# Kernel optimization log

Measured on AMD Instinct MI355X. Metric: run time of the kernel, lower is better.

Reference implementation:

```python
import jax, jax.numpy as jnp
import numpy as np

B, S, D, H = 2, 2048, 1024, 16
DK = D // H
NEG = -1e9


def setup_inputs() -> dict:
    key = jax.random.key(0)
    ks = jax.random.split(key, 12)
    sc = 1.0 / np.sqrt(D)
    inp = {
        "query": jax.random.normal(ks[0], (B, S, D), jnp.float32),
        "key": jax.random.normal(ks[1], (B, S, D), jnp.float32),
        "value": jax.random.normal(ks[2], (B, S, D), jnp.float32),
        "mask": jnp.ones((B, 1, S), jnp.int32),
        "Wq": jax.random.normal(ks[3], (D, D), jnp.float32) * sc,
        "bq": jnp.zeros((D,), jnp.float32),
        "Wk": jax.random.normal(ks[4], (D, D), jnp.float32) * sc,
        "bk": jnp.zeros((D,), jnp.float32),
        "Wv": jax.random.normal(ks[5], (D, D), jnp.float32) * sc,
        "bv": jnp.zeros((D,), jnp.float32),
        "Wo": jax.random.normal(ks[6], (D, D), jnp.float32) * sc,
        "bo": jnp.zeros((D,), jnp.float32),
    }
    return inp


def reference(query, key, value, mask, Wq, bq, Wk, bk, Wv, bv, Wo, bo):
    # projections + split heads: [B,S,D] -> [B,H,S,DK]
    def proj(x, W, b):
        return (x @ W + b).reshape(B, S, H, DK).transpose(0, 2, 1, 3)

    q = proj(query, Wq, bq)
    k = proj(key, Wk, bk)
    v = proj(value, Wv, bv)

    scores = jnp.einsum("bhqd,bhkd->bhqk", q, k) / jnp.sqrt(jnp.float32(DK))
    # mask: [B,1,S] -> unsqueeze head dim -> [B,1,1,S], broadcast over heads & queries
    m = mask[:, None, :, :]  # [B,1,1,S]
    scores = jnp.where(m == 0, NEG, scores)
    p_attn = jax.nn.softmax(scores, axis=-1)  # dropout p=0 (eval)
    x = jnp.einsum("bhqk,bhkd->bhqd", p_attn, v)
    x = x.transpose(0, 2, 1, 3).reshape(B, S, D)
    return x @ Wo + bo
```

## Files before the change

kernel.cpp:

```cpp
#include <hip/hip_runtime.h>
#include <stdint.h>

typedef unsigned short u16;
typedef __bf16 bf16x8 __attribute__((ext_vector_type(8), may_alias));
typedef unsigned short u16x8 __attribute__((ext_vector_type(8), may_alias));
typedef unsigned short u16x4 __attribute__((ext_vector_type(4), may_alias));
typedef float f32x4 __attribute__((ext_vector_type(4)));
typedef float f32x16 __attribute__((ext_vector_type(16)));

__device__ __forceinline__ u16 f2bf(float f) {
    union { float f; uint32_t i; } v; v.f = f;
    return (u16)((v.i + 0x7FFFu + ((v.i >> 16) & 1u)) >> 16);
}

__device__ __forceinline__ float exp2_hw(float x) {
#if __has_builtin(__builtin_amdgcn_exp2f)
    return __builtin_amdgcn_exp2f(x);
#else
    float r; asm("v_exp_f32 %0, %1" : "=v"(r) : "v"(x)); return r;
#endif
}

__device__ __forceinline__ uint32_t cvt_pk_bf16(float a, float b) {
    uint32_t r;
    asm("v_cvt_pk_bf16_f32 %0, %1, %2" : "=v"(r) : "v"(a), "v"(b));
    return r;
}

__device__ __forceinline__ void gld_lds16(const u16* g, u16* l) {
    __builtin_amdgcn_global_load_lds(
        (const __attribute__((address_space(1))) unsigned int*)g,
        (__attribute__((address_space(3))) unsigned int*)l, 16, 0, 0);
}

__global__ __launch_bounds__(256) void cvt_all(
    const float* __restrict__ s0, const float* __restrict__ s1, const float* __restrict__ s2,
    const float* __restrict__ w0, const float* __restrict__ w1,
    const float* __restrict__ w2, const float* __restrict__ w3,
    u16* __restrict__ d0, u16* __restrict__ d1, u16* __restrict__ d2,
    u16* __restrict__ t0, u16* __restrict__ t1,
    u16* __restrict__ t2, u16* __restrict__ t3)
{
    __shared__ float L[64][65];
    const int z = blockIdx.z;
    const int tid = threadIdx.x;
    if (z < 3) {
        const float* s = (z == 0) ? s0 : (z == 1) ? s1 : s2;
        u16*         d = (z == 0) ? d0 : (z == 1) ? d1 : d2;
        const size_t base = ((size_t)blockIdx.x * 256 + tid) * 16;
        #pragma unroll
        for (int p = 0; p < 2; ++p) {
            float4 a = *reinterpret_cast<const float4*>(s + base + p * 8);
            float4 b = *reinterpret_cast<const float4*>(s + base + p * 8 + 4);
            u16x8 o;
            o[0] = f2bf(a.x); o[1] = f2bf(a.y); o[2] = f2bf(a.z); o[3] = f2bf(a.w);
            o[4] = f2bf(b.x); o[5] = f2bf(b.y); o[6] = f2bf(b.z); o[7] = f2bf(b.w);
            *reinterpret_cast<u16x8*>(d + base + p * 8) = o;
        }
    } else {
        if (blockIdx.x >= 256) return;
        const int zi = z - 3;
        const float* w = (zi == 0) ? w0 : (zi == 1) ? w1 : (zi == 2) ? w2 : w3;
        u16*         t = (zi == 0) ? t0 : (zi == 1) ? t1 : (zi == 2) ? t2 : t3;
        const int k0 = (blockIdx.x & 15) * 64, n0 = (blockIdx.x >> 4) * 64;
        const int rr = tid >> 6, cc = tid & 63;
        #pragma unroll
        for (int p = 0; p < 16; ++p)
            L[p * 4 + rr][cc] = w[(size_t)(k0 + p * 4 + rr) * 1024 + n0 + cc];
        __syncthreads();
        #pragma unroll
        for (int p = 0; p < 16; ++p)
            t[(size_t)(n0 + p * 4 + rr) * 1024 + k0 + cc] = f2bf(L[cc][p * 4 + rr]);
    }
}

__global__ __launch_bounds__(256) void gemm_bt(
    const u16* __restrict__ A0, const u16* __restrict__ A1, const u16* __restrict__ A2,
    const u16* __restrict__ B0, const u16* __restrict__ B1, const u16* __restrict__ B2,
    const float* __restrict__ c0, const float* __restrict__ c1, const float* __restrict__ c2,
    void* __restrict__ d0, void* __restrict__ d1, void* __restrict__ d2,
    int mode_override)
{
    __shared__ u16 As[2 * 4096];
    __shared__ u16 Bs[2 * 4096];

    const int z = blockIdx.z;
    const u16* A = (z == 0) ? A0 : (z == 1) ? A1 : A2;
    const u16* BT = (z == 0) ? B0 : (z == 1) ? B1 : B2;
    const float* bias = (z == 0) ? c0 : (z == 1) ? c1 : c2;
    void* dst = (z == 0) ? d0 : (z == 1) ? d1 : d2;
    const int mode = (mode_override >= 0) ? mode_override : ((z == 2) ? 2 : 0);

    const int tid  = threadIdx.x;
    const int wave = tid >> 6, lane = tid & 63;
    const int quad = lane >> 4, l15 = lane & 15;
    const int row0 = blockIdx.x * 128, col0 = blockIdx.y * 128;
    const int wrow = (wave >> 1) * 64, wcol = (wave & 1) * 64;

    const int sidx0 = tid, sidx1 = 256 + tid;
    const int sr0 = sidx0 >> 2, sc0 = ((sidx0 & 3) ^ ((sr0 >> 1) & 3)) * 8;
    const int sr1 = sidx1 >> 2, sc1 = ((sidx1 & 3) ^ ((sr1 >> 1) & 3)) * 8;
    const size_t aoff0 = (size_t)(row0 + sr0) * 1024 + sc0;
    const size_t aoff1 = (size_t)(row0 + sr1) * 1024 + sc1;
    const size_t boff0 = (size_t)(col0 + sr0) * 1024 + sc0;
    const size_t boff1 = (size_t)(col0 + sr1) * 1024 + sc1;
    u16* const asl0 = &As[(size_t)(wave * 64) * 8];
    u16* const asl1 = &As[(size_t)(256 + wave * 64) * 8];
    u16* const bsl0 = &Bs[(size_t)(wave * 64) * 8];
    u16* const bsl1 = &Bs[(size_t)(256 + wave * 64) * 8];

    f32x4 acc[4][4] = {};

    gld_lds16(A + aoff0, asl0);
    gld_lds16(BT + boff0, bsl0);
    gld_lds16(A + aoff1, asl1);
    gld_lds16(BT + boff1, bsl1);
    __syncthreads();

    int cur = 0;
    for (int k0 = 0; k0 < 1024; k0 += 32) {
        if (k0 < 992) {
            const int nb = (cur ^ 1) * 4096;
            gld_lds16(A + aoff0 + (k0 + 32), asl0 + nb);
            gld_lds16(BT + boff0 + (k0 + 32), bsl0 + nb);
            gld_lds16(A + aoff1 + (k0 + 32), asl1 + nb);
            gld_lds16(BT + boff1 + (k0 + 32), bsl1 + nb);
        }

        const u16* Ab = &As[cur * 4096];
        const u16* Bb = &Bs[cur * 4096];
        bf16x8 a[4], b[4];
        #pragma unroll
        for (int i = 0; i < 4; ++i) {
            const int ar = wrow + i * 16 + l15;
            a[i] = *reinterpret_cast<const bf16x8*>(&Ab[ar * 32 + (quad ^ ((ar >> 1) & 3)) * 8]);
        }
        #pragma unroll
        for (int j = 0; j < 4; ++j) {
            const int br = wcol + j * 16 + l15;
            b[j] = *reinterpret_cast<const bf16x8*>(&Bb[br * 32 + (quad ^ ((br >> 1) & 3)) * 8]);
        }
        #pragma unroll
        for (int i = 0; i < 4; ++i)
            #pragma unroll
            for (int j = 0; j < 4; ++j)
                acc[i][j] = __builtin_amdgcn_mfma_f32_16x16x32_bf16(a[i], b[j], acc[i][j], 0, 0, 0);

        __syncthreads();
        cur ^= 1;
    }

    const float emul = (mode == 0 && z == 0 && mode_override < 0) ? 0.18033688011112042f : 1.0f;

    #pragma unroll
    for (int i = 0; i < 4; ++i) {
        #pragma unroll
        for (int j = 0; j < 4; ++j) {
            const int gc  = col0 + wcol + j * 16 + l15;
            const float bv = bias[gc];
            const int gr0 = row0 + wrow + i * 16 + quad * 4;
            if (mode == 3) {
                float* df = (float*)dst;
                #pragma unroll
                for (int r = 0; r < 4; ++r)
                    df[(size_t)(gr0 + r) * 1024 + gc] = acc[i][j][r] + bv;
            } else if (mode == 2) {
                u16* dp = (u16*)dst;
                const int b = gr0 >> 11, s = gr0 & 2047;
                const int h = gc >> 6,  dk = gc & 63;
                u16x4 pk;
                pk[0] = f2bf(acc[i][j][0] + bv);
                pk[1] = f2bf(acc[i][j][1] + bv);
                pk[2] = f2bf(acc[i][j][2] + bv);
                pk[3] = f2bf(acc[i][j][3] + bv);
                *reinterpret_cast<u16x4*>(dp + ((size_t)((b * 16 + h) * 64 + dk)) * 2048 + s) = pk;
            } else {
                u16* dp = (u16*)dst;
                #pragma unroll
                for (int r = 0; r < 4; ++r) {
                    const int gr = gr0 + r;
                    const int b = gr >> 11, s = gr & 2047;
                    const int h = gc >> 6, dk = gc & 63;
                    dp[((size_t)((b * 16 + h) * 2048 + s)) * 64 + dk] = f2bf((acc[i][j][r] + bv) * emul);
                }
            }
        }
    }
}

__global__ __launch_bounds__(512, 4) void attn_fused(
    const u16* __restrict__ Qb, const u16* __restrict__ Kb,
    const u16* __restrict__ Vt, const int* __restrict__ mask,
    u16* __restrict__ ctx)
{
    __shared__ __align__(16) u16 SMEM[16896];

    const int tid  = threadIdx.x;
    const int w    = tid >> 6;
    const int lane = tid & 63;
    const int l31  = lane & 31;
    const int hi   = lane >> 5;
    const int qw   = w & 3;
    const int kh   = w >> 2;

    const int id = blockIdx.x;
    const int sw = (id & 7) * 64 + (id >> 3);
    const int bh = sw >> 4;
    const int q0 = (sw & 15) * 128;
    const int b  = bh >> 4, h = bh & 15;

    const u16* Qp = Qb + (size_t)bh * 2048 * 64;
    const u16* Kp = Kb + (size_t)bh * 2048 * 64;
    const u16* Vp = Vt + (size_t)bh * 64 * 2048;
    const int* mp = mask + b * 2048;

    bf16x8 qf[4];
    {
        const u16* qrow = Qp + (size_t)(q0 + qw * 32 + l31) * 64 + hi * 8;
        #pragma unroll
        for (int s = 0; s < 4; ++s)
            qf[s] = *reinterpret_cast<const bf16x8*>(qrow + s * 16);
    }

    const int scb = tid & 7, sr = tid >> 3;
    const u16* kg0 = Kp + (size_t)sr * 64 + scb * 8;
    const u16* vg0 = Vp + (size_t)sr * 2048 + scb * 8;
    const int dK = scb * 512 + (sr ^ scb) * 8;

    {
        u16x8 kr = *reinterpret_cast<const u16x8*>(kg0);
        u16x8 vr = *reinterpret_cast<const u16x8*>(vg0);
        *reinterpret_cast<u16x8*>(&SMEM[dK])        = kr;
        *reinterpret_cast<u16x8*>(&SMEM[4096 + dK]) = vr;
    }
    int mreg = mp[lane];
    __syncthreads();

    f32x16 accO0 = {}, accO1 = {};
    float la0 = 0.f, la1 = 0.f, la2 = 0.f, la3 = 0.f;
    const int paddr = (lane ^ 32) << 2;

    int cur = 0;
    for (int t = 0; t < 32; ++t) {
        const int kk = t * 64;
        u16x8 krn, vrn; int mnext = 1;
        if (t < 31) {
            krn = *reinterpret_cast<const u16x8*>(kg0 + (size_t)(kk + 64) * 64);
            vrn = *reinterpret_cast<const u16x8*>(vg0 + (kk + 64));
            mnext = mp[kk + 64 + lane];
        }
        const u16* Kb_ = &SMEM[cur * 8192];
        const u16* Vb_ = &SMEM[cur * 8192 + 4096];

        const bool fullmask = (__ballot(mreg != 0) == ~0ull);

        f32x16 z = {};
        #pragma unroll
        for (int s = 0; s < 4; ++s) {
            const int cb = s * 2 + hi;
            const bf16x8 ak = *reinterpret_cast<const bf16x8*>(
                &Kb_[cb * 512 + (((kh * 32 + l31)) ^ cb) * 8]);
            z = __builtin_amdgcn_mfma_f32_32x32x16_bf16(ak, qf[s], z, 0, 0, 0);
        }
        float p[16];
        #pragma unroll
        for (int r = 0; r < 16; ++r) p[r] = exp2_hw(z[r]);
        if (!fullmask) {
            #pragma unroll
            for (int r = 0; r < 16; ++r) {
                const int kv = kk + kh * 32 + (r & 3) + 8 * (r >> 2) + 4 * hi;
                if (mp[kv] == 0) p[r] = 0.f;
            }
        }
        la0 += p[0] + p[4] + p[8]  + p[12];
        la1 += p[1] + p[5] + p[9]  + p[13];
        la2 += p[2] + p[6] + p[10] + p[14];
        la3 += p[3] + p[7] + p[11] + p[15];

        const uint32_t wd0 = cvt_pk_bf16(p[0],  p[1]);
        const uint32_t wd1 = cvt_pk_bf16(p[2],  p[3]);
        const uint32_t wd2 = cvt_pk_bf16(p[4],  p[5]);
        const uint32_t wd3 = cvt_pk_bf16(p[6],  p[7]);
        const uint32_t wd4 = cvt_pk_bf16(p[8],  p[9]);
        const uint32_t wd5 = cvt_pk_bf16(p[10], p[11]);
        const uint32_t wd6 = cvt_pk_bf16(p[12], p[13]);
        const uint32_t wd7 = cvt_pk_bf16(p[14], p[15]);
        const uint32_t s0 = hi ? wd0 : wd2;
        const uint32_t s1 = hi ? wd1 : wd3;
        const uint32_t s2 = hi ? wd4 : wd6;
        const uint32_t s3 = hi ? wd5 : wd7;
        const uint32_t r0 = (uint32_t)__builtin_amdgcn_ds_bpermute(paddr, (int)s0);
        const uint32_t r1 = (uint32_t)__builtin_amdgcn_ds_bpermute(paddr, (int)s1);
        const uint32_t r2 = (uint32_t)__builtin_amdgcn_ds_bpermute(paddr, (int)s2);
        const uint32_t r3 = (uint32_t)__builtin_amdgcn_ds_bpermute(paddr, (int)s3);
        union { uint32_t u[4]; bf16x8 v; } A0, A1;
        A0.u[0] = hi ? r0  : wd0;
        A0.u[1] = hi ? r1  : wd1;
        A0.u[2] = hi ? wd2 : r0;
        A0.u[3] = hi ? wd3 : r1;
        A1.u[0] = hi ? r2  : wd4;
        A1.u[1] = hi ? r3  : wd5;
        A1.u[2] = hi ? wd6 : r2;
        A1.u[3] = hi ? wd7 : r3;

        const int ck0 = kh * 4 + hi;
        const int ck1 = kh * 4 + 2 + hi;
        const bf16x8 bv00 = *reinterpret_cast<const bf16x8*>(&Vb_[ck0 * 512 + ((     l31) ^ ck0) * 8]);
        const bf16x8 bv01 = *reinterpret_cast<const bf16x8*>(&Vb_[ck1 * 512 + ((     l31) ^ ck1) * 8]);
        const bf16x8 bv10 = *reinterpret_cast<const bf16x8*>(&Vb_[ck0 * 512 + ((32 + l31) ^ ck0) * 8]);
        const bf16x8 bv11 = *reinterpret_cast<const bf16x8*>(&Vb_[ck1 * 512 + ((32 + l31) ^ ck1) * 8]);
        accO0 = __builtin_amdgcn_mfma_f32_32x32x16_bf16(A0.v, bv00, accO0, 0, 0, 0);
        accO0 = __builtin_amdgcn_mfma_f32_32x32x16_bf16(A1.v, bv01, accO0, 0, 0, 0);
        accO1 = __builtin_amdgcn_mfma_f32_32x32x16_bf16(A0.v, bv10, accO1, 0, 0, 0);
        accO1 = __builtin_amdgcn_mfma_f32_32x32x16_bf16(A1.v, bv11, accO1, 0, 0, 0);

        if (t < 31) {
            const int nb = (cur ^ 1) * 8192;
            *reinterpret_cast<u16x8*>(&SMEM[nb + dK])        = krn;
            *reinterpret_cast<u16x8*>(&SMEM[nb + 4096 + dK]) = vrn;
        }
        __syncthreads();
        cur ^= 1;
        mreg = mnext;
    }

    float l_part = (la0 + la1) + (la2 + la3);
    l_part += __shfl_xor(l_part, 32);
    float* F = (float*)SMEM;
    if (kh) {
        #pragma unroll
        for (int r = 0; r < 16; ++r) F[qw * 1024 + r * 64 + lane] = accO0[r];
        #pragma unroll
        for (int r = 0; r < 16; ++r) F[4096 + qw * 1024 + r * 64 + lane] = accO1[r];
        if (lane < 32) F[8192 + qw * 32 + l31] = l_part;
    }
    __syncthreads();
    if (!kh && lane < 32)
        F[8320 + qw * 32 + l31] = 1.0f / (l_part + F[8192 + qw * 32 + l31]);
    __syncthreads();
    if (!kh) {
        #pragma unroll
        for (int r = 0; r < 16; ++r) {
            const int qr = (r & 3) + 8 * (r >> 2) + 4 * hi;
            const float iv = F[8320 + qw * 32 + qr];
            const float o0 = accO0[r] + F[qw * 1024 + r * 64 + lane];
            const float o1 = accO1[r] + F[4096 + qw * 1024 + r * 64 + lane];
            u16* row = ctx + (size_t)(b * 2048 + q0 + qw * 32 + qr) * 1024 + h * 64;
            row[l31]      = f2bf(o0 * iv);
            row[32 + l31] = f2bf(o1 * iv);
        }
    }
}

extern "C" void kernel_launch(void* const* d_in, const int* in_sizes, int n_in,
                              void* d_out, int out_size, void* d_ws, size_t ws_size,
                              hipStream_t stream) {
    const float* query = (const float*)d_in[0];
    const float* key   = (const float*)d_in[1];
    const float* value = (const float*)d_in[2];
    const int*   mask  = (const int*)d_in[3];
    const float* Wq = (const float*)d_in[4];
    const float* bq = (const float*)d_in[5];
    const float* Wk = (const float*)d_in[6];
    const float* bk = (const float*)d_in[7];
    const float* Wv = (const float*)d_in[8];
    const float* bv = (const float*)d_in[9];
    const float* Wo = (const float*)d_in[10];
    const float* bo = (const float*)d_in[11];
    float* out = (float*)d_out;

    u16* ws   = (u16*)d_ws;
    u16* Xq   = ws;
    u16* Xk   = ws + 4194304;
    u16* Xv   = ws + 8388608;
    u16* WqT  = ws + 12582912;
    u16* WkT  = ws + 13631488;
    u16* WvT  = ws + 14680064;
    u16* WoT  = ws + 15728640;
    u16* Qb   = ws + 16777216;
    u16* Kb   = ws + 20971520;
    u16* Vt   = ws + 25165824;
    u16* ctx  = Xq;

    dim3 blk(256);
    cvt_all<<<dim3(1024, 1, 7), blk, 0, stream>>>(query, key, value, Wq, Wk, Wv, Wo,
                                                  Xq, Xk, Xv, WqT, WkT, WvT, WoT);
    gemm_bt<<<dim3(32, 8, 3),  blk, 0, stream>>>(Xq, Xk, Xv, WqT, WkT, WvT,
                                                 bq, bk, bv, Qb, Kb, Vt, -1);
    attn_fused<<<dim3(512), dim3(512), 0, stream>>>(Qb, Kb, Vt, mask, ctx);
    gemm_bt<<<dim3(32, 8, 1),  blk, 0, stream>>>(ctx, ctx, ctx, WoT, WoT, WoT,
                                                 bo, bo, bo, out, out, out, 3);
}
```

Before: 224.8 us.

## Use direct global-to-LDS K/V loads, permlane32 swap, and MFMA priority hints

Replaces the register-staged K/V tile prefetch with global_load_lds direct-to-LDS copies issued at the top of each iteration into the other buffer, with each wave writing one swizzled column block. This removes VGPR staging and explicit LDS stores. It also swaps the four ds_bpermute exchanges plus selects for v_permlane32_swap, and brackets the MFMA groups with s_setprio to favour matrix issue. The new LDS layout relies on the direct-load addressing matching the old XOR swizzle, and there is a risk of missing vmcnt waits before the barrier.

```diff
diff --git a/kernel.cpp b/kernel.cpp
--- a/kernel.cpp
+++ b/kernel.cpp
@@ -7,6 +7,7 @@
 typedef unsigned short u16x4 __attribute__((ext_vector_type(4), may_alias));
 typedef float f32x4 __attribute__((ext_vector_type(4)));
 typedef float f32x16 __attribute__((ext_vector_type(16)));
+typedef int i32x2 __attribute__((ext_vector_type(2)));
 
 __device__ __forceinline__ u16 f2bf(float f) {
     union { float f; uint32_t i; } v; v.f = f;
@@ -25,6 +26,15 @@
     uint32_t r;
     asm("v_cvt_pk_bf16_f32 %0, %1, %2" : "=v"(r) : "v"(a), "v"(b));
     return r;
+}
+
+__device__ __forceinline__ void pl32swap(uint32_t& a, uint32_t& b) {
+#if __has_builtin(__builtin_amdgcn_permlane32_swap)
+    i32x2 r = __builtin_amdgcn_permlane32_swap((int)a, (int)b, false, false);
+    a = (uint32_t)r[0]; b = (uint32_t)r[1];
+#else
+    asm("v_permlane32_swap_b32 %0, %1" : "+v"(a), "+v"(b));
+#endif
 }
 
 __device__ __forceinline__ void gld_lds16(const u16* g, u16* l) {
@@ -222,31 +232,25 @@
             qf[s] = *reinterpret_cast<const bf16x8*>(qrow + s * 16);
     }
 
-    const int scb = tid & 7, sr = tid >> 3;
-    const u16* kg0 = Kp + (size_t)sr * 64 + scb * 8;
-    const u16* vg0 = Vp + (size_t)sr * 2048 + scb * 8;
-    const int dK = scb * 512 + (sr ^ scb) * 8;
-
-    {
-        u16x8 kr = *reinterpret_cast<const u16x8*>(kg0);
-        u16x8 vr = *reinterpret_cast<const u16x8*>(vg0);
-        *reinterpret_cast<u16x8*>(&SMEM[dK])        = kr;
-        *reinterpret_cast<u16x8*>(&SMEM[4096 + dK]) = vr;
-    }
+    const u16* kgs = Kp + (size_t)(lane ^ w) * 64 + w * 8;
+    const u16* vgs = Vp + (size_t)(lane ^ w) * 2048 + w * 8;
+
+    gld_lds16(kgs, &SMEM[w * 512]);
+    gld_lds16(vgs, &SMEM[4096 + w * 512]);
     int mreg = mp[lane];
     __syncthreads();
 
     f32x16 accO0 = {}, accO1 = {};
     float la0 = 0.f, la1 = 0.f, la2 = 0.f, la3 = 0.f;
-    const int paddr = (lane ^ 32) << 2;
 
     int cur = 0;
     for (int t = 0; t < 32; ++t) {
         const int kk = t * 64;
-        u16x8 krn, vrn; int mnext = 1;
+        int mnext = 1;
         if (t < 31) {
-            krn = *reinterpret_cast<const u16x8*>(kg0 + (size_t)(kk + 64) * 64);
-            vrn = *reinterpret_cast<const u16x8*>(vg0 + (kk + 64));
+            const int nb = (cur ^ 1) * 8192;
+            gld_lds16(kgs + (size_t)(kk + 64) * 64, &SMEM[nb + w * 512]);
+            gld_lds16(vgs + (kk + 64), &SMEM[nb + 4096 + w * 512]);
             mnext = mp[kk + 64 + lane];
         }
         const u16* Kb_ = &SMEM[cur * 8192];
@@ -255,6 +259,7 @@
         const bool fullmask = (__ballot(mreg != 0) == ~0ull);
 
         f32x16 z = {};
+        __builtin_amdgcn_s_setprio(1);
         #pragma unroll
         for (int s = 0; s < 4; ++s) {
             const int cb = s * 2 + hi;
@@ -262,6 +267,7 @@
                 &Kb_[cb * 512 + (((kh * 32 + l31)) ^ cb) * 8]);
             z = __builtin_amdgcn_mfma_f32_32x32x16_bf16(ak, qf[s], z, 0, 0, 0);
         }
+        __builtin_amdgcn_s_setprio(0);
         float p[16];
         #pragma unroll
         for (int r = 0; r < 16; ++r) p[r] = exp2_hw(z[r]);
@@ -277,31 +283,21 @@
         la2 += p[2] + p[6] + p[10] + p[14];
         la3 += p[3] + p[7] + p[11] + p[15];
 
-        const uint32_t wd0 = cvt_pk_bf16(p[0],  p[1]);
-        const uint32_t wd1 = cvt_pk_bf16(p[2],  p[3]);
-        const uint32_t wd2 = cvt_pk_bf16(p[4],  p[5]);
-        const uint32_t wd3 = cvt_pk_bf16(p[6],  p[7]);
-        const uint32_t wd4 = cvt_pk_bf16(p[8],  p[9]);
-        const uint32_t wd5 = cvt_pk_bf16(p[10], p[11]);
-        const uint32_t wd6 = cvt_pk_bf16(p[12], p[13]);
-        const uint32_t wd7 = cvt_pk_bf16(p[14], p[15]);
-        const uint32_t s0 = hi ? wd0 : wd2;
-        const uint32_t s1 = hi ? wd1 : wd3;
-        const uint32_t s2 = hi ? wd4 : wd6;
-        const uint32_t s3 = hi ? wd5 : wd7;
-        const uint32_t r0 = (uint32_t)__builtin_amdgcn_ds_bpermute(paddr, (int)s0);
-        const uint32_t r1 = (uint32_t)__builtin_amdgcn_ds_bpermute(paddr, (int)s1);
-        const uint32_t r2 = (uint32_t)__builtin_amdgcn_ds_bpermute(paddr, (int)s2);
-        const uint32_t r3 = (uint32_t)__builtin_amdgcn_ds_bpermute(paddr, (int)s3);
+        uint32_t wd0 = cvt_pk_bf16(p[0],  p[1]);
+        uint32_t wd1 = cvt_pk_bf16(p[2],  p[3]);
+        uint32_t wd2 = cvt_pk_bf16(p[4],  p[5]);
+        uint32_t wd3 = cvt_pk_bf16(p[6],  p[7]);
+        uint32_t wd4 = cvt_pk_bf16(p[8],  p[9]);
+        uint32_t wd5 = cvt_pk_bf16(p[10], p[11]);
+        uint32_t wd6 = cvt_pk_bf16(p[12], p[13]);
+        uint32_t wd7 = cvt_pk_bf16(p[14], p[15]);
+        pl32swap(wd0, wd2);
+        pl32swap(wd1, wd3);
+        pl32swap(wd4, wd6);
+        pl32swap(wd5, wd7);
         union { uint32_t u[4]; bf16x8 v; } A0, A1;
-        A0.u[0] = hi ? r0  : wd0;
-        A0.u[1] = hi ? r1  : wd1;
-        A0.u[2] = hi ? wd2 : r0;
-        A0.u[3] = hi ? wd3 : r1;
-        A1.u[0] = hi ? r2  : wd4;
-        A1.u[1] = hi ? r3  : wd5;
-        A1.u[2] = hi ? wd6 : r2;
-        A1.u[3] = hi ? wd7 : r3;
+        A0.u[0] = wd0; A0.u[1] = wd1; A0.u[2] = wd2; A0.u[3] = wd3;
+        A1.u[0] = wd4; A1.u[1] = wd5; A1.u[2] = wd6; A1.u[3] = wd7;
 
         const int ck0 = kh * 4 + hi;
         const int ck1 = kh * 4 + 2 + hi;
@@ -309,16 +305,13 @@
         const bf16x8 bv01 = *reinterpret_cast<const bf16x8*>(&Vb_[ck1 * 512 + ((     l31) ^ ck1) * 8]);
         const bf16x8 bv10 = *reinterpret_cast<const bf16x8*>(&Vb_[ck0 * 512 + ((32 + l31) ^ ck0) * 8]);
         const bf16x8 bv11 = *reinterpret_cast<const bf16x8*>(&Vb_[ck1 * 512 + ((32 + l31) ^ ck1) * 8]);
+        __builtin_amdgcn_s_setprio(1);
         accO0 = __builtin_amdgcn_mfma_f32_32x32x16_bf16(A0.v, bv00, accO0, 0, 0, 0);
         accO0 = __builtin_amdgcn_mfma_f32_32x32x16_bf16(A1.v, bv01, accO0, 0, 0, 0);
         accO1 = __builtin_amdgcn_mfma_f32_32x32x16_bf16(A0.v, bv10, accO1, 0, 0, 0);
         accO1 = __builtin_amdgcn_mfma_f32_32x32x16_bf16(A1.v, bv11, accO1, 0, 0, 0);
-
-        if (t < 31) {
-            const int nb = (cur ^ 1) * 8192;
-            *reinterpret_cast<u16x8*>(&SMEM[nb + dK])        = krn;
-            *reinterpret_cast<u16x8*>(&SMEM[nb + 4096 + dK]) = vrn;
-        }
+        __builtin_amdgcn_s_setprio(0);
+
         __syncthreads();
         cur ^= 1;
         mreg = mnext;
```

New measurement: 226.0 us, median of 2. Within noise of the previous version (+0.5%).
